# Kernel tuning notes

Hardware: AMD Instinct MI355X
Metric: run time of the kernel (lower is better)

## Reference

```python
import jax, jax.numpy as jnp
import numpy as np

V, BLK, L, H, E = 50257, 1024, 12, 12, 768
HS = E // H
B = 2


def _ln(x, w, b, eps=1e-5):
    mu = jnp.mean(x, axis=-1, keepdims=True)
    var = jnp.mean((x - mu) ** 2, axis=-1, keepdims=True)
    return (x - mu) * jax.lax.rsqrt(var + eps) * w + b


def setup_inputs() -> dict:
    key = jax.random.key(0)
    ks = jax.random.split(key, 16)
    s = 0.02
    inp = {
        "x": jax.random.randint(ks[0], (B, BLK), 0, V),
        "tok_emb": jax.random.normal(ks[1], (V, E), jnp.float32) * s,
        "pos_emb": jax.random.normal(ks[2], (BLK, E), jnp.float32) * s,
        "qW": jax.random.normal(ks[3], (L, H, HS, E), jnp.float32) * s,
        "kW": jax.random.normal(ks[4], (L, H, HS, E), jnp.float32) * s,
        "vW": jax.random.normal(ks[5], (L, H, HS, E), jnp.float32) * s,
        "ln1_w": jnp.ones((L, E), jnp.float32),
        "ln1_b": jnp.zeros((L, E), jnp.float32),
        "fc1_w": jax.random.normal(ks[6], (L, 4 * E, E), jnp.float32) * s,
        "fc1_b": jnp.zeros((L, 4 * E), jnp.float32),
        "fc2_w": jax.random.normal(ks[7], (L, E, 4 * E), jnp.float32) * s,
        "fc2_b": jnp.zeros((L, E), jnp.float32),
        "ln2_w": jnp.ones((L, E), jnp.float32),
        "ln2_b": jnp.zeros((L, E), jnp.float32),
        "lnf_w": jnp.ones((E,), jnp.float32),
        "lnf_b": jnp.zeros((E,), jnp.float32),
        "lm_w": jax.random.normal(ks[8], (V, E), jnp.float32) * s,
    }
    return inp


def _gpt(x, tok_emb, pos_emb, qW, kW, vW, ln1_w, ln1_b, fc1_w, fc1_b,
         fc2_w, fc2_b, ln2_w, ln2_b, lnf_w, lnf_b, lm_w):
    T = x.shape[1]
    h = tok_emb[x] + pos_emb[None, :T]  # [B,T,E]
    scale = 1.0 / jnp.sqrt(jnp.asarray(E, h.dtype))  # C**0.5 with C=n_embd
    causal = jnp.tril(jnp.ones((T, T), bool))  # mask where tril==0
    for l in range(L):
        q = jnp.einsum("bte,hde->bthd", h, qW[l])
        k = jnp.einsum("bte,hde->bthd", h, kW[l])
        v = jnp.einsum("bte,hde->bthd", h, vW[l])
        # faithful to source: w = k @ q^T / sqrt(n_embd); rows index k, cols index q
        w = jnp.einsum("bshd,bthd->bhst", k, q) * scale
        w = jnp.where(causal[None, None], w, -jnp.inf)
        w = jax.nn.softmax(w, axis=-1)
        a = jnp.einsum("bhst,bthd->bshd", w, v)  # [B,T,H,HS]
        a = a.reshape(a.shape[0], T, E)  # head-major concat
        h = _ln(h + a, ln1_w[l], ln1_b[l])
        m = jax.nn.gelu(jnp.einsum("bte,fe->btf", h, fc1_w[l]) + fc1_b[l],
                        approximate=False)
        m = jnp.einsum("btf,ef->bte", m, fc2_w[l]) + fc2_b[l]
        h = _ln(h + m, ln2_w[l], ln2_b[l])
    h = _ln(h, lnf_w, lnf_b)
    return jnp.einsum("bte,ve->btv", h, lm_w)


def reference(x, tok_emb, pos_emb, qW, kW, vW, ln1_w, ln1_b, fc1_w, fc1_b,
              fc2_w, fc2_b, ln2_w, ln2_b, lnf_w, lnf_b, lm_w):
    return _gpt(x, tok_emb, pos_emb, qW, kW, vW, ln1_w, ln1_b, fc1_w, fc1_b,
                fc2_w, fc2_b, ln2_w, ln2_b, lnf_w, lnf_b, lm_w)
```

## Files before the change

### kernel.cpp

```cpp
#include <hip/hip_runtime.h>
#include <math.h>

typedef unsigned short u16;
typedef __attribute__((ext_vector_type(8))) short short8;
typedef __attribute__((ext_vector_type(8))) u16 ushort8_t;
typedef __attribute__((ext_vector_type(4))) u16 ushort4_t;
typedef __attribute__((ext_vector_type(4))) float f32x4;

#define BB 2
#define TT 1024
#define EE 768
#define HH 12
#define HSZ 64
#define LL 12
#define FF 3072
#define VV 50257
#define VPAD 50304
#define MM 2048
#define NQKV 2304
#define QKW 1536
#define KVB 128
#define BK 64

__device__ __forceinline__ float bf2f(u16 u) {
    union { unsigned int i; float f; } c;
    c.i = ((unsigned int)u) << 16;
    return c.f;
}
__device__ __forceinline__ u16 f2bf(float f) {
    unsigned int u = __float_as_uint(f);
    unsigned int r = (u + 0x7FFFu + ((u >> 16) & 1u)) >> 16;
    return (u16)r;
}

__device__ __forceinline__ void gload_lds16(const void* g, void* l) {
    __builtin_amdgcn_global_load_lds(
        (const __attribute__((address_space(1))) unsigned int*)g,
        (__attribute__((address_space(3))) unsigned int*)l,
        16, 0, 0);
}

template<int N> __device__ __forceinline__ void waitcnt_vm() {
    if      constexpr (N == 0)  asm volatile("s_waitcnt vmcnt(0)" ::: "memory");
    else if constexpr (N == 4)  asm volatile("s_waitcnt vmcnt(4)" ::: "memory");
    else if constexpr (N == 6)  asm volatile("s_waitcnt vmcnt(6)" ::: "memory");
    else if constexpr (N == 8)  asm volatile("s_waitcnt vmcnt(8)" ::: "memory");
    else if constexpr (N == 12) asm volatile("s_waitcnt vmcnt(12)" ::: "memory");
    else static_assert(N == 0, "unsupported vmcnt");
}

__device__ __forceinline__ void xcd_swizzle(int& bx, int& by) {
    int nx = gridDim.x;
    int nwg = nx * gridDim.y;
    int orig = blockIdx.x + blockIdx.y * nx;
    int q = nwg >> 3, r = nwg & 7;
    int xcd = orig & 7, idx = orig >> 3;
    int nf = (xcd < r ? xcd * (q + 1) : r * (q + 1) + (xcd - r) * q) + idx;
    bx = nf % nx;
    by = nf / nx;
}

__global__ __launch_bounds__(256)
void cast_all_kernel(const float* __restrict__ qW, const float* __restrict__ kW,
                     const float* __restrict__ vW, const float* __restrict__ fc1w,
                     const float* __restrict__ fc2w, const float* __restrict__ lmw,
                     u16* __restrict__ wqkv, u16* __restrict__ wfc1,
                     u16* __restrict__ wfc2, u16* __restrict__ wlm)
{
    const int j = blockIdx.y;
    const float* s;
    u16* d;
    long total, per, stride;
    switch (j) {
    case 0: s = qW;   d = wqkv;              total = (long)LL * EE * EE; per = (long)EE * EE; stride = (long)NQKV * EE; break;
    case 1: s = kW;   d = wqkv + EE * EE;     total = (long)LL * EE * EE; per = (long)EE * EE; stride = (long)NQKV * EE; break;
    case 2: s = vW;   d = wqkv + 2 * EE * EE; total = (long)LL * EE * EE; per = (long)EE * EE; stride = (long)NQKV * EE; break;
    case 3: s = fc1w; d = wfc1;              total = (long)LL * FF * EE; per = total; stride = total; break;
    case 4: s = fc2w; d = wfc2;              total = (long)LL * EE * FF; per = total; stride = total; break;
    default: s = lmw; d = wlm;               total = (long)VV * EE;      per = total; stride = total; break;
    }
    long step = (long)gridDim.x * blockDim.x * 4;
    for (long i = ((long)blockIdx.x * blockDim.x + threadIdx.x) * 4; i < total; i += step) {
        long layer = i / per;
        long off = i - layer * per;
        float4 v = *reinterpret_cast<const float4*>(s + i);
        ushort4_t o;
        o[0] = f2bf(v.x); o[1] = f2bf(v.y); o[2] = f2bf(v.z); o[3] = f2bf(v.w);
        *reinterpret_cast<ushort4_t*>(d + layer * stride + off) = o;
    }
}

__global__ void embed_kernel(const int* __restrict__ x, const float* __restrict__ tok,
                             const float* __restrict__ pos, float* __restrict__ h,
                             u16* __restrict__ hb)
{
    int row = blockIdx.x;
    int t = row & (TT - 1);
    int id = x[row];
    const float* tr = tok + (size_t)id * EE;
    const float* pr = pos + (size_t)t * EE;
    for (int i = threadIdx.x; i < EE; i += blockDim.x) {
        float v = tr[i] + pr[i];
        h[(size_t)row * EE + i] = v;
        hb[(size_t)row * EE + i] = f2bf(v);
    }
}

__global__ __launch_bounds__(256)
void add_ln_kernel(const float* __restrict__ hin, const float* __restrict__ add,
                   const float* __restrict__ w, const float* __restrict__ bias,
                   float* __restrict__ hout, u16* __restrict__ hbout)
{
    int lane = threadIdx.x & 63, wv = threadIdx.x >> 6;
    int row = blockIdx.x * 4 + wv;
    const float* hp = hin + (size_t)row * EE;
    float x[12];
    float s = 0.f;
#pragma unroll
    for (int c = 0; c < 3; ++c) {
        float4 hv = *reinterpret_cast<const float4*>(hp + c * 256 + lane * 4);
        if (add) {
            float4 av = *reinterpret_cast<const float4*>(add + (size_t)row * EE + c * 256 + lane * 4);
            hv.x += av.x; hv.y += av.y; hv.z += av.z; hv.w += av.w;
        }
        x[c * 4 + 0] = hv.x; x[c * 4 + 1] = hv.y; x[c * 4 + 2] = hv.z; x[c * 4 + 3] = hv.w;
        s += hv.x + hv.y + hv.z + hv.w;
    }
#pragma unroll
    for (int o = 32; o > 0; o >>= 1) s += __shfl_xor(s, o);
    float mu = s * (1.0f / EE);
    float vs = 0.f;
#pragma unroll
    for (int i = 0; i < 12; ++i) { float d = x[i] - mu; vs += d * d; }
#pragma unroll
    for (int o = 32; o > 0; o >>= 1) vs += __shfl_xor(vs, o);
    float inv = 1.0f / sqrtf(vs * (1.0f / EE) + 1e-5f);
#pragma unroll
    for (int c = 0; c < 3; ++c) {
        int col = c * 256 + lane * 4;
        float4 wv4 = *reinterpret_cast<const float4*>(w + col);
        float4 bv4 = *reinterpret_cast<const float4*>(bias + col);
        float4 o;
        o.x = (x[c * 4 + 0] - mu) * inv * wv4.x + bv4.x;
        o.y = (x[c * 4 + 1] - mu) * inv * wv4.y + bv4.y;
        o.z = (x[c * 4 + 2] - mu) * inv * wv4.z + bv4.z;
        o.w = (x[c * 4 + 3] - mu) * inv * wv4.w + bv4.w;
        *reinterpret_cast<float4*>(hout + (size_t)row * EE + col) = o;
        ushort4_t ob;
        ob[0] = f2bf(o.x); ob[1] = f2bf(o.y); ob[2] = f2bf(o.z); ob[3] = f2bf(o.w);
        *reinterpret_cast<ushort4_t*>(hbout + (size_t)row * EE + col) = ob;
    }
}

enum { EPI_GELU_BF16 = 1, EPI_BIAS_F32 = 2, EPI_F32 = 3, EPI_QKV = 4 };

template<int EPI, bool NGUARD, int DEPTH, int WM, int WN, int MR, int NR>
__global__ __launch_bounds__(WM * WN * 64, 2)
void gemm_kernel(const u16* __restrict__ A, const u16* __restrict__ Bw,
                 const float* __restrict__ bias, void* __restrict__ Cout,
                 void* __restrict__ vTout, int Ndim, int Kdim)
{
    constexpr int NW  = WM * WN;
    constexpr int BMT = WM * MR * 16;
    constexpr int BNT = WN * NR * 16;
    constexpr int CA  = BMT / (8 * NW);
    constexpr int CB  = BNT / (8 * NW);
    constexpr int NLD = CA + CB;
    static_assert(BMT % (8 * NW) == 0 && BNT % (8 * NW) == 0, "stage geom");
    __shared__ u16 As[DEPTH * BMT * BK];
    __shared__ u16 Bs[DEPTH * BNT * BK];
    const int tid = threadIdx.x;
    const int lane = tid & 63;
    const int wid = tid >> 6;
    const int wm = wid / WN, wn = wid % WN;
    int bx, by;
    xcd_swizzle(bx, by);
    const int rowBase = bx * BMT;
    const int colBase = by * BNT;

    const int srow = lane >> 3;
    const int scol = ((lane & 7) ^ srow) * 8;

#define GSTAGE(k0_, buf_)                                                         \
    {                                                                             \
        _Pragma("unroll")                                                         \
        for (int i_ = 0; i_ < CA; ++i_) {                                         \
            int r0_ = (wid * CA + i_) * 8;                                        \
            gload_lds16(A + (size_t)(rowBase + r0_ + srow) * Kdim + (k0_) + scol, \
                        As + (buf_) * (BMT * BK) + r0_ * BK);                     \
        }                                                                         \
        _Pragma("unroll")                                                         \
        for (int i_ = 0; i_ < CB; ++i_) {                                         \
            int r0_ = (wid * CB + i_) * 8;                                        \
            gload_lds16(Bw + (size_t)(colBase + r0_ + srow) * Kdim + (k0_) + scol,\
                        Bs + (buf_) * (BNT * BK) + r0_ * BK);                     \
        }                                                                         \
    }

#define COMPUTE(Asb_, Bsb_)                                                       \
    {                                                                             \
        const int fr = lane & 15;                                                 \
        const int qd = lane >> 4;                                                 \
        _Pragma("unroll")                                                         \
        for (int kk = 0; kk < 2; ++kk) {                                          \
            short8 af[MR], bfr[NR];                                               \
            int goff = (((kk * 4 + qd) ^ (fr & 7))) * 8;                          \
            _Pragma("unroll")                                                     \
            for (int mi = 0; mi < MR; ++mi)                                       \
                af[mi] = *reinterpret_cast<const short8*>(                        \
                    &(Asb_)[(wm * (MR * 16) + mi * 16 + fr) * BK + goff]);        \
            _Pragma("unroll")                                                     \
            for (int ni = 0; ni < NR; ++ni)                                       \
                bfr[ni] = *reinterpret_cast<const short8*>(                       \
                    &(Bsb_)[(wn * (NR * 16) + ni * 16 + fr) * BK + goff]);        \
            _Pragma("unroll")                                                     \
            for (int mi = 0; mi < MR; ++mi)                                       \
                _Pragma("unroll")                                                 \
                for (int ni = 0; ni < NR; ++ni)                                   \
                    acc[mi][ni] = __builtin_amdgcn_mfma_f32_16x16x32_bf16(        \
                        af[mi], bfr[ni], acc[mi][ni], 0, 0, 0);                   \
        }                                                                         \
    }

    f32x4 acc[MR][NR] = {};
    const int nk = Kdim / BK;

    if (DEPTH > 1) {
#pragma unroll
        for (int p = 0; p < DEPTH; ++p) GSTAGE(p * BK, p)
        int cur = 0;
        for (int t = 0; t < nk; ++t) {
            int rem = nk - 1 - t;
            if (rem >= DEPTH - 1)            waitcnt_vm<NLD * (DEPTH - 1)>();
            else if (DEPTH > 2 && rem == 1)  waitcnt_vm<NLD>();
            else                             waitcnt_vm<0>();
            __builtin_amdgcn_s_barrier();
            const u16* Asb = As + cur * (BMT * BK);
            const u16* Bsb = Bs + cur * (BNT * BK);
            COMPUTE(Asb, Bsb)
            __builtin_amdgcn_s_barrier();
            if (t + DEPTH < nk) GSTAGE((t + DEPTH) * BK, cur)
            cur = (cur + 1 == DEPTH) ? 0 : cur + 1;
        }
    } else {
        for (int t = 0; t < nk; ++t) {
            GSTAGE(t * BK, 0)
            __syncthreads();
            COMPUTE(As, Bs)
            __syncthreads();
        }
    }

    if (EPI == EPI_QKV && colBase >= QKW) {
        u16* T = Bs;
        __syncthreads();
#pragma unroll
        for (int mi = 0; mi < MR; ++mi)
#pragma unroll
            for (int ni = 0; ni < NR; ++ni)
#pragma unroll
                for (int r = 0; r < 4; ++r) {
                    int lr = wm * (MR * 16) + mi * 16 + (lane >> 4) * 4 + r;
                    int lc = wn * (NR * 16) + ni * 16 + (lane & 15);
                    T[lc * 72 + lr] = f2bf(acc[mi][ni][r]);
                }
        __syncthreads();
        constexpr int SEGS = BMT / 32;
        int hdl = tid / SEGS;
        int seg = (tid % SEGS) * 32;
        if (hdl < BNT) {
            int b_ = rowBase >> 10;
            int t0 = rowBase & (TT - 1);
            u16* dst = (u16*)vTout + ((size_t)b_ * EE + (colBase - QKW) + hdl) * TT + t0 + seg;
            const u16* src = T + hdl * 72 + seg;
#pragma unroll
            for (int j = 0; j < 4; ++j)
                *reinterpret_cast<ushort8_t*>(dst + j * 8) =
                    *reinterpret_cast<const ushort8_t*>(src + j * 8);
        }
        return;
    }

#pragma unroll
    for (int mi = 0; mi < MR; ++mi) {
#pragma unroll
        for (int ni = 0; ni < NR; ++ni) {
#pragma unroll
            for (int r = 0; r < 4; ++r) {
                int row = rowBase + wm * (MR * 16) + mi * 16 + (lane >> 4) * 4 + r;
                int col = colBase + wn * (NR * 16) + ni * 16 + (lane & 15);
                if (NGUARD && col >= Ndim) continue;
                float v = acc[mi][ni][r];
                if (EPI == EPI_GELU_BF16) { v += bias[col]; v = 0.5f * v * (1.0f + erff(v * 0.70710678f)); }
                if (EPI == EPI_BIAS_F32)  { v += bias[col]; }
                size_t idx = (size_t)row * Ndim + col;
                if (EPI == EPI_QKV) {
                    ((u16*)Cout)[(size_t)row * QKW + col] = f2bf(v);
                } else if (EPI == EPI_GELU_BF16) {
                    ((u16*)Cout)[idx] = f2bf(v);
                } else {
                    ((float*)Cout)[idx] = v;
                }
            }
        }
    }
}

__global__ __launch_bounds__(256)
void attn_kernel(const u16* __restrict__ qkb, const u16* __restrict__ vT,
                 float* __restrict__ aout)
{
    __shared__ u16 Qs[2 * KVB * 64];
    __shared__ u16 Vs[2 * 64 * KVB];
    __shared__ u16 Ps[4 * 16 * KVB];

    const int lane = threadIdx.x & 63;
    const int wv = threadIdx.x >> 6;
    int bxs, bys;
    xcd_swizzle(bxs, bys);
    const int js = (gridDim.x - 1) - bxs;
    const int s0 = js * 64;
    const int smax = s0 + 63;
    const int bh = bys;
    const int b = bh / HH, h = bh % HH;
    const int bT = b * TT;
    const float scale = 0.036084392f;

    short8 af[2];
    {
        int srow = bT + s0 + wv * 16 + (lane & 15);
#pragma unroll
        for (int kk = 0; kk < 2; ++kk)
            af[kk] = *reinterpret_cast<const short8*>(
                qkb + (size_t)srow * QKW + EE + h * HSZ + kk * 32 + (lane >> 4) * 8);
    }

    const int ntiles = (s0 + 63) / KVB + 1;
    const int qrow = lane >> 3;
    const int qu = lane & 7;
    const int vrow = lane >> 4;
    const int vu = lane & 15;

#define ASTAGE(jt2_, buf_)                                                            \
    {                                                                                 \
        int tb_ = (jt2_) * KVB;                                                       \
        _Pragma("unroll")                                                             \
        for (int i_ = 0; i_ < 4; ++i_) {                                              \
            int R0_ = wv * 32 + i_ * 8;                                               \
            int row_ = R0_ + qrow;                                                    \
            gload_lds16(qkb + (size_t)(bT + tb_ + row_) * QKW + h * HSZ               \
                            + ((qu ^ (row_ & 7)) * 8),                                \
                        &Qs[(buf_) * (KVB * 64) + R0_ * 64]);                         \
        }                                                                             \
        _Pragma("unroll")                                                             \
        for (int i_ = 0; i_ < 4; ++i_) {                                              \
            int R0_ = wv * 16 + i_ * 4;                                               \
            int row_ = R0_ + vrow;                                                    \
            gload_lds16(vT + ((size_t)b * EE + h * HSZ + row_) * TT + tb_             \
                            + ((vu ^ (row_ & 15)) * 8),                               \
                        &Vs[(buf_) * (64 * KVB) + R0_ * KVB]);                        \
        }                                                                             \
    }

    ASTAGE(0, 0)

    float m[4], l[4];
    f32x4 oacc[4] = {};
#pragma unroll
    for (int r = 0; r < 4; ++r) { m[r] = -INFINITY; l[r] = 0.f; }

    int cur = 0;
    for (int jt2 = 0; jt2 < ntiles; ++jt2) {
        __syncthreads();
        if (jt2 + 1 < ntiles) ASTAGE(jt2 + 1, cur ^ 1)

        const u16* Qb = &Qs[cur * (KVB * 64)];
        const u16* Vb = &Vs[cur * (64 * KVB)];
        const int tb = jt2 * KVB;
        const int navail = smax - tb;
        const int nact = min(8, (navail >> 4) + 1);
        const int nkc  = min(4, (navail >> 5) + 1);
        const bool dg = (tb + KVB - 1 > s0);

        f32x4 sc[8];
#pragma unroll
        for (int ni = 0; ni < 8; ++ni) {
            if (ni < nact) {
                f32x4 a = {};
                int trow = ni * 16 + (lane & 15);
#pragma unroll
                for (int kk = 0; kk < 2; ++kk) {
                    int g = kk * 4 + (lane >> 4);
                    short8 bq = *reinterpret_cast<const short8*>(
                        &Qb[trow * 64 + ((g ^ (trow & 7)) * 8)]);
                    a = __builtin_amdgcn_mfma_f32_16x16x32_bf16(af[kk], bq, a, 0, 0, 0);
                }
                sc[ni] = a;
            } else {
                f32x4 mn = {-1e30f, -1e30f, -1e30f, -1e30f};
                sc[ni] = mn;
            }
        }

        if (dg) {
#pragma unroll
            for (int ni = 0; ni < 8; ++ni)
#pragma unroll
                for (int r = 0; r < 4; ++r) {
                    float sv = sc[ni][r] * scale;
                    int t = tb + ni * 16 + (lane & 15);
                    int s = s0 + wv * 16 + (lane >> 4) * 4 + r;
                    if (t > s) sv = -1e30f;
                    sc[ni][r] = sv;
                }
        } else {
#pragma unroll
            for (int ni = 0; ni < 8; ++ni)
#pragma unroll
                for (int r = 0; r < 4; ++r) sc[ni][r] *= scale;
        }

        f32x4 pexp[8];
#pragma unroll
        for (int r = 0; r < 4; ++r) {
            float rm = sc[0][r];
#pragma unroll
            for (int ni = 1; ni < 8; ++ni) rm = fmaxf(rm, sc[ni][r]);
#pragma unroll
            for (int o = 1; o < 16; o <<= 1) rm = fmaxf(rm, __shfl_xor(rm, o));
            float mnew = fmaxf(m[r], rm);
            float alpha = __expf(m[r] - mnew);
            m[r] = mnew;
            float rs = 0.f;
#pragma unroll
            for (int ni = 0; ni < 8; ++ni) {
                float p;
                if (ni < nact) p = __expf(sc[ni][r] - mnew);
                else p = 0.f;
                pexp[ni][r] = p;
                rs += p;
            }
#pragma unroll
            for (int o = 1; o < 16; o <<= 1) rs += __shfl_xor(rs, o);
            l[r] = l[r] * alpha + rs;
#pragma unroll
            for (int dt = 0; dt < 4; ++dt) oacc[dt][r] *= alpha;
        }

        const int nst = nkc * 2;
#pragma unroll
        for (int ni = 0; ni < 8; ++ni) {
            if (ni < nst) {
#pragma unroll
                for (int r = 0; r < 4; ++r) {
                    int sl = (lane >> 4) * 4 + r;
                    int tl = ni * 16 + (lane & 15);
                    Ps[wv * (16 * KVB) + sl * KVB + (((tl >> 3) ^ sl) & 15) * 8 + (tl & 7)]
                        = f2bf(pexp[ni][r]);
                }
            }
        }

#pragma unroll
        for (int kc = 0; kc < 4; ++kc) {
            if (kc < nkc) {
                int srow = lane & 15;
                int g = kc * 4 + (lane >> 4);
                short8 pa = *reinterpret_cast<const short8*>(
                    &Ps[wv * (16 * KVB) + srow * KVB + ((g ^ srow) & 15) * 8]);
#pragma unroll
                for (int dt = 0; dt < 4; ++dt) {
                    int drow = dt * 16 + (lane & 15);
                    short8 bv = *reinterpret_cast<const short8*>(
                        &Vb[drow * KVB + (((kc * 4 + (lane >> 4)) ^ drow) & 15) * 8]);
                    oacc[dt] = __builtin_amdgcn_mfma_f32_16x16x32_bf16(pa, bv, oacc[dt], 0, 0, 0);
                }
            }
        }
        cur ^= 1;
    }

    float invl[4];
#pragma unroll
    for (int r = 0; r < 4; ++r) invl[r] = 1.0f / l[r];
#pragma unroll
    for (int dt = 0; dt < 4; ++dt)
#pragma unroll
        for (int r = 0; r < 4; ++r) {
            int sg = s0 + wv * 16 + (lane >> 4) * 4 + r;
            aout[(size_t)(bT + sg) * EE + h * HSZ + dt * 16 + (lane & 15)] =
                oacc[dt][r] * invl[r];
        }
}

extern "C" void kernel_launch(void* const* d_in, const int* in_sizes, int n_in,
                              void* d_out, int out_size, void* d_ws, size_t ws_size,
                              hipStream_t stream)
{
    const int*   x    = (const int*)d_in[0];
    const float* tok  = (const float*)d_in[1];
    const float* pos  = (const float*)d_in[2];
    const float* qW   = (const float*)d_in[3];
    const float* kW   = (const float*)d_in[4];
    const float* vW   = (const float*)d_in[5];
    const float* ln1w = (const float*)d_in[6];
    const float* ln1b = (const float*)d_in[7];
    const float* fc1w = (const float*)d_in[8];
    const float* fc1b = (const float*)d_in[9];
    const float* fc2w = (const float*)d_in[10];
    const float* fc2b = (const float*)d_in[11];
    const float* ln2w = (const float*)d_in[12];
    const float* ln2b = (const float*)d_in[13];
    const float* lnfw = (const float*)d_in[14];
    const float* lnfb = (const float*)d_in[15];
    const float* lmw  = (const float*)d_in[16];
    float* out = (float*)d_out;

    char* ws = (char*)d_ws;
    u16* wqkv = (u16*)ws;  ws += (size_t)LL * NQKV * EE * 2;
    u16* wfc1 = (u16*)ws;  ws += (size_t)LL * FF * EE * 2;
    u16* wfc2 = (u16*)ws;  ws += (size_t)LL * EE * FF * 2;
    u16* wlm  = (u16*)ws;  ws += (size_t)VPAD * EE * 2;
    float* h    = (float*)ws; ws += (size_t)MM * EE * 4;
    float* tmp  = (float*)ws; ws += (size_t)MM * EE * 4;
    u16* qkb = (u16*)ws;      ws += (size_t)MM * QKW * 2;
    u16* vTb = (u16*)ws;      ws += (size_t)BB * EE * TT * 2;
    u16* hb  = (u16*)ws;      ws += (size_t)MM * EE * 2;
    u16* mb  = (u16*)ws;      ws += (size_t)MM * FF * 2;

    dim3 blk(256);

    cast_all_kernel<<<dim3(1024, 6), blk, 0, stream>>>(
        qW, kW, vW, fc1w, fc2w, lmw, wqkv, wfc1, wfc2, wlm);

    embed_kernel<<<MM, blk, 0, stream>>>(x, tok, pos, h, hb);

    dim3 gQKV(MM / 64, NQKV / 128);
    dim3 gF1(MM / 64, FF / 128);
    dim3 gF2(MM / 64, EE / 64);
    dim3 gV(MM / 256, VPAD / 128);
    dim3 gAttn(TT / 64, BB * HH);

    for (int l = 0; l < LL; ++l) {
        gemm_kernel<EPI_QKV, false, 2, 2, 2, 2, 4><<<gQKV, blk, 0, stream>>>(
            hb, wqkv + (size_t)l * NQKV * EE, nullptr, qkb, vTb, NQKV, EE);
        attn_kernel<<<gAttn, blk, 0, stream>>>(qkb, vTb, tmp);
        add_ln_kernel<<<MM / 4, blk, 0, stream>>>(h, tmp, ln1w + l * EE, ln1b + l * EE, h, hb);
        gemm_kernel<EPI_GELU_BF16, false, 2, 2, 2, 2, 4><<<gF1, blk, 0, stream>>>(
            hb, wfc1 + (size_t)l * FF * EE, fc1b + (size_t)l * FF, mb, nullptr, FF, EE);
        gemm_kernel<EPI_BIAS_F32, false, 3, 2, 2, 2, 2><<<gF2, blk, 0, stream>>>(
            mb, wfc2 + (size_t)l * EE * FF, fc2b + (size_t)l * EE, tmp, nullptr, EE, FF);
        add_ln_kernel<<<MM / 4, blk, 0, stream>>>(h, tmp, ln2w + l * EE, ln2b + l * EE, h, hb);
    }
    add_ln_kernel<<<MM / 4, blk, 0, stream>>>(h, nullptr, lnfw, lnfb, h, hb);
    gemm_kernel<EPI_F32, true, 1, 4, 2, 4, 4><<<gV, dim3(512), 0, stream>>>(
        hb, wlm, nullptr, out, nullptr, VV, EE);
}
```

Measured before the change: 1.958 ms.

## Split-K the FC2 GEMM into two partials and retile the LM-head GEMM

The FC2 GEMM (K=3072, N=768) now runs as a 2-way split-K across blockIdx.z. Each half writes its own fp32 partial buffer, and the following add+LayerNorm kernel sums both partials with the residual. This doubles the block count of a GEMM that otherwise launches few tiles, at the cost of writing and reading an extra fp32 activation buffer. Separately, the LM-head GEMM switches from a 512-thread 256-row tile to a 256-thread 128-row tile. That halves the tile and doubles the grid, trading some reuse for more parallelism.

```diff
diff --git a/kernel.cpp b/kernel.cpp
--- a/kernel.cpp
+++ b/kernel.cpp
@@ -108,6 +108,7 @@
 
 __global__ __launch_bounds__(256)
 void add_ln_kernel(const float* __restrict__ hin, const float* __restrict__ add,
+                   const float* __restrict__ add2,
                    const float* __restrict__ w, const float* __restrict__ bias,
                    float* __restrict__ hout, u16* __restrict__ hbout)
 {
@@ -121,6 +122,10 @@
         float4 hv = *reinterpret_cast<const float4*>(hp + c * 256 + lane * 4);
         if (add) {
             float4 av = *reinterpret_cast<const float4*>(add + (size_t)row * EE + c * 256 + lane * 4);
+            hv.x += av.x; hv.y += av.y; hv.z += av.z; hv.w += av.w;
+        }
+        if (add2) {
+            float4 av = *reinterpret_cast<const float4*>(add2 + (size_t)row * EE + c * 256 + lane * 4);
             hv.x += av.x; hv.y += av.y; hv.z += av.z; hv.w += av.w;
         }
         x[c * 4 + 0] = hv.x; x[c * 4 + 1] = hv.y; x[c * 4 + 2] = hv.z; x[c * 4 + 3] = hv.w;
@@ -154,11 +159,11 @@
 
 enum { EPI_GELU_BF16 = 1, EPI_BIAS_F32 = 2, EPI_F32 = 3, EPI_QKV = 4 };
 
-template<int EPI, bool NGUARD, int DEPTH, int WM, int WN, int MR, int NR>
+template<int EPI, bool NGUARD, int DEPTH, int WM, int WN, int MR, int NR, bool KSPLIT = false>
 __global__ __launch_bounds__(WM * WN * 64, 2)
 void gemm_kernel(const u16* __restrict__ A, const u16* __restrict__ Bw,
                  const float* __restrict__ bias, void* __restrict__ Cout,
-                 void* __restrict__ vTout, int Ndim, int Kdim)
+                 void* __restrict__ vTout, int Ndim, int Kdim, int Kstride)
 {
     constexpr int NW  = WM * WN;
     constexpr int BMT = WM * MR * 16;
@@ -178,23 +183,26 @@
     const int rowBase = bx * BMT;
     const int colBase = by * BNT;
 
+    const u16* Ab = A + (KSPLIT ? (size_t)blockIdx.z * Kdim : 0);
+    const u16* Bb = Bw + (KSPLIT ? (size_t)blockIdx.z * Kdim : 0);
+
     const int srow = lane >> 3;
     const int scol = ((lane & 7) ^ srow) * 8;
 
-#define GSTAGE(k0_, buf_)                                                         \
-    {                                                                             \
-        _Pragma("unroll")                                                         \
-        for (int i_ = 0; i_ < CA; ++i_) {                                         \
-            int r0_ = (wid * CA + i_) * 8;                                        \
-            gload_lds16(A + (size_t)(rowBase + r0_ + srow) * Kdim + (k0_) + scol, \
-                        As + (buf_) * (BMT * BK) + r0_ * BK);                     \
-        }                                                                         \
-        _Pragma("unroll")                                                         \
-        for (int i_ = 0; i_ < CB; ++i_) {                                         \
-            int r0_ = (wid * CB + i_) * 8;                                        \
-            gload_lds16(Bw + (size_t)(colBase + r0_ + srow) * Kdim + (k0_) + scol,\
-                        Bs + (buf_) * (BNT * BK) + r0_ * BK);                     \
-        }                                                                         \
+#define GSTAGE(k0_, buf_)                                                          \
+    {                                                                              \
+        _Pragma("unroll")                                                          \
+        for (int i_ = 0; i_ < CA; ++i_) {                                          \
+            int r0_ = (wid * CA + i_) * 8;                                         \
+            gload_lds16(Ab + (size_t)(rowBase + r0_ + srow) * Kstride + (k0_) + scol, \
+                        As + (buf_) * (BMT * BK) + r0_ * BK);                      \
+        }                                                                          \
+        _Pragma("unroll")                                                          \
+        for (int i_ = 0; i_ < CB; ++i_) {                                          \
+            int r0_ = (wid * CB + i_) * 8;                                         \
+            gload_lds16(Bb + (size_t)(colBase + r0_ + srow) * Kstride + (k0_) + scol, \
+                        Bs + (buf_) * (BNT * BK) + r0_ * BK);                      \
+        }                                                                          \
     }
 
 #define COMPUTE(Asb_, Bsb_)                                                       \
@@ -281,6 +289,7 @@
         return;
     }
 
+    const size_t zoff = KSPLIT ? (size_t)blockIdx.z * MM * Ndim : 0;
 #pragma unroll
     for (int mi = 0; mi < MR; ++mi) {
 #pragma unroll
@@ -292,14 +301,14 @@
                 if (NGUARD && col >= Ndim) continue;
                 float v = acc[mi][ni][r];
                 if (EPI == EPI_GELU_BF16) { v += bias[col]; v = 0.5f * v * (1.0f + erff(v * 0.70710678f)); }
-                if (EPI == EPI_BIAS_F32)  { v += bias[col]; }
+                if (EPI == EPI_BIAS_F32)  { if (!KSPLIT || blockIdx.z == 0) v += bias[col]; }
                 size_t idx = (size_t)row * Ndim + col;
                 if (EPI == EPI_QKV) {
                     ((u16*)Cout)[(size_t)row * QKW + col] = f2bf(v);
                 } else if (EPI == EPI_GELU_BF16) {
                     ((u16*)Cout)[idx] = f2bf(v);
                 } else {
-                    ((float*)Cout)[idx] = v;
+                    ((float*)Cout)[zoff + idx] = v;
                 }
             }
         }
@@ -522,7 +531,8 @@
     u16* wfc2 = (u16*)ws;  ws += (size_t)LL * EE * FF * 2;
     u16* wlm  = (u16*)ws;  ws += (size_t)VPAD * EE * 2;
     float* h    = (float*)ws; ws += (size_t)MM * EE * 4;
-    float* tmp  = (float*)ws; ws += (size_t)MM * EE * 4;
+    float* tmp  = (float*)ws; ws += (size_t)2 * MM * EE * 4;
+    float* tmp2 = tmp + (size_t)MM * EE;
     u16* qkb = (u16*)ws;      ws += (size_t)MM * QKW * 2;
     u16* vTb = (u16*)ws;      ws += (size_t)BB * EE * TT * 2;
     u16* hb  = (u16*)ws;      ws += (size_t)MM * EE * 2;
@@ -537,22 +547,25 @@
 
     dim3 gQKV(MM / 64, NQKV / 128);
     dim3 gF1(MM / 64, FF / 128);
-    dim3 gF2(MM / 64, EE / 64);
-    dim3 gV(MM / 256, VPAD / 128);
+    dim3 gF2(MM / 64, EE / 64, 2);
+    dim3 gV(MM / 128, VPAD / 128);
     dim3 gAttn(TT / 64, BB * HH);
 
     for (int l = 0; l < LL; ++l) {
         gemm_kernel<EPI_QKV, false, 2, 2, 2, 2, 4><<<gQKV, blk, 0, stream>>>(
-            hb, wqkv + (size_t)l * NQKV * EE, nullptr, qkb, vTb, NQKV, EE);
+            hb, wqkv + (size_t)l * NQKV * EE, nullptr, qkb, vTb, NQKV, EE, EE);
         attn_kernel<<<gAttn, blk, 0, stream>>>(qkb, vTb, tmp);
-        add_ln_kernel<<<MM / 4, blk, 0, stream>>>(h, tmp, ln1w + l * EE, ln1b + l * EE, h, hb);
+        add_ln_kernel<<<MM / 4, blk, 0, stream>>>(h, tmp, nullptr,
+                                                  ln1w + l * EE, ln1b + l * EE, h, hb);
         gemm_kernel<EPI_GELU_BF16, false, 2, 2, 2, 2, 4><<<gF1, blk, 0, stream>>>(
-            hb, wfc1 + (size_t)l * FF * EE, fc1b + (size_t)l * FF, mb, nullptr, FF, EE);
-        gemm_kernel<EPI_BIAS_F32, false, 3, 2, 2, 2, 2><<<gF2, blk, 0, stream>>>(
-            mb, wfc2 + (size_t)l * EE * FF, fc2b + (size_t)l * EE, tmp, nullptr, EE, FF);
-        add_ln_kernel<<<MM / 4, blk, 0, stream>>>(h, tmp, ln2w + l * EE, ln2b + l * EE, h, hb);
-    }
-    add_ln_kernel<<<MM / 4, blk, 0, stream>>>(h, nullptr, lnfw, lnfb, h, hb);
-    gemm_kernel<EPI_F32, true, 1, 4, 2, 4, 4><<<gV, dim3(512), 0, stream>>>(
-        hb, wlm, nullptr, out, nullptr, VV, EE);
-}
+            hb, wfc1 + (size_t)l * FF * EE, fc1b + (size_t)l * FF, mb, nullptr, FF, EE, EE);
+        gemm_kernel<EPI_BIAS_F32, false, 3, 2, 2, 2, 2, true><<<gF2, blk, 0, stream>>>(
+            mb, wfc2 + (size_t)l * EE * FF, fc2b + (size_t)l * EE, tmp, nullptr,
+            EE, FF / 2, FF);
+        add_ln_kernel<<<MM / 4, blk, 0, stream>>>(h, tmp, tmp2,
+                                                  ln2w + l * EE, ln2b + l * EE, h, hb);
+    }
+    add_ln_kernel<<<MM / 4, blk, 0, stream>>>(h, nullptr, nullptr, lnfw, lnfb, h, hb);
+    gemm_kernel<EPI_F32, true, 1, 2, 2, 4, 4><<<gV, blk, 0, stream>>>(
+        hb, wlm, nullptr, out, nullptr, VV, EE, EE);
+}
```

New measurement: 1.733 ms. 11.5% less time.
